# Performance work log

Measured on AMD Instinct MI355X. Metric: run time of the kernel, lower is better.

The kernel has to match this reference:

```python
import jax, jax.numpy as jnp
import numpy as np

H = W = 224
NOISE_STD = 0.45
BRIGHTNESS = 1.1          # uniform(0.8, 1.2) in original
ANGLE_DEG = 10.0          # randint(-20, 21) in original
CROP_I, CROP_J, CROP_SZ = 32, 32, 160

# Perspective: startpoints (input corners) -> endpoints (output corners).
STARTPOINTS = [[0, 0], [223, 0], [223, 223], [0, 223]]
ENDPOINTS = [[30, 20], [200, 25], [210, 200], [15, 190]]  # fixed draws within original ranges

def _perspective_coeffs(startpoints, endpoints):
    # Solve homography mapping OUTPUT coords (endpoints) -> INPUT coords (startpoints),
    # same convention as torchvision._get_perspective_coeffs(endpoints, startpoints).
    A = np.zeros((8, 8), dtype=np.float64)
    b = np.zeros((8,), dtype=np.float64)
    for k, ((xi, yi), (xo, yo)) in enumerate(zip(startpoints, endpoints)):
        A[2 * k] = [xo, yo, 1, 0, 0, 0, -xo * xi, -yo * xi]
        b[2 * k] = xi
        A[2 * k + 1] = [0, 0, 0, xo, yo, 1, -xo * yi, -yo * yi]
        b[2 * k + 1] = yi
    return np.linalg.solve(A, b)  # a,b,c,d,e,f,g,h

COEFFS = _perspective_coeffs(STARTPOINTS, ENDPOINTS)

def bilinear_sample(img, src_x, src_y):
    # img: [B,C,H,W]; src_x/src_y: [Ho,Wo] source pixel coords; zero fill outside.
    Hh, Ww = img.shape[-2], img.shape[-1]
    x0 = jnp.floor(src_x); y0 = jnp.floor(src_y)
    wx1 = src_x - x0; wx0 = 1.0 - wx1
    wy1 = src_y - y0; wy0 = 1.0 - wy1
    def gather(yi, xi):
        valid = (xi >= 0) & (xi <= Ww - 1) & (yi >= 0) & (yi <= Hh - 1)
        xc = jnp.clip(xi, 0, Ww - 1).astype(jnp.int32)
        yc = jnp.clip(yi, 0, Hh - 1).astype(jnp.int32)
        return img[:, :, yc, xc] * valid.astype(img.dtype)
    return (gather(y0, x0) * (wy0 * wx0) + gather(y0, x0 + 1) * (wy0 * wx1)
            + gather(y0 + 1, x0) * (wy1 * wx0) + gather(y0 + 1, x0 + 1) * (wy1 * wx1))

def perspective_grid():
    a, b_, c, d, e, f, g, h = [float(v) for v in COEFFS]
    yo, xo = jnp.meshgrid(jnp.arange(H, dtype=jnp.float32), jnp.arange(W, dtype=jnp.float32), indexing='ij')
    denom = g * xo + h * yo + 1.0
    return (a * xo + b_ * yo + c) / denom, (d * xo + e * yo + f) / denom

def rotate_grid(angle_deg):
    cx, cy = (W - 1) / 2.0, (H - 1) / 2.0
    t = jnp.float32(np.deg2rad(angle_deg))
    cos, sin = jnp.cos(t), jnp.sin(t)
    yo, xo = jnp.meshgrid(jnp.arange(H, dtype=jnp.float32), jnp.arange(W, dtype=jnp.float32), indexing='ij')
    dx, dy = xo - cx, yo - cy
    return cx + cos * dx + sin * dy, cy - sin * dx + cos * dy

def setup_inputs() -> dict:
    key = jax.random.key(0)
    k1, k2 = jax.random.split(key)
    x = jax.random.uniform(k1, (128, 3, H, W), dtype=jnp.float32)
    noise = jax.random.normal(k2, (128, 3, H, W), dtype=jnp.float32)
    return {"x": x, "noise": noise}

def reference(x, noise):
    # (hflip result discarded in the original -> no-op)
    x = x + NOISE_STD * noise                       # additive gaussian noise
    x = jnp.clip(x * BRIGHTNESS, 0.0, 1.0)          # adjust_brightness (float clamp to [0,1])
    px, py = perspective_grid()
    x = bilinear_sample(x, px, py)                  # perspective warp, bilinear, fill 0
    rx, ry = rotate_grid(ANGLE_DEG)
    x = bilinear_sample(x, rx, ry)                  # rotate, bilinear, fill 0
    x = x[..., CROP_I:CROP_I + CROP_SZ, CROP_J:CROP_J + CROP_SZ]  # 160x160 crop
    B, C = x.shape[0], x.shape[1]
    x = jax.image.resize(x, (B, C, H, W), method='bicubic')       # bicubic upsample back to 224
    return x
```

## Files before the change

### kernel.cpp

```cpp
#include <hip/hip_runtime.h>
#include <cmath>
#include <cstring>

#define HH 224
#define WW 224
#define CROP 160
#define CI 32
#define CJ 32
#define NCH 384
#define CH_STRIDE (HH*WW)
#define CROP_STRIDE (CROP*CROP)

#define TILE2 32
#define NTIL2 5
#define GCH2 8
#define BH2 64
#define BHCAP 62
#define NG2 18
#define BWSTR 77

#define TILE 16
#define NTIL 10
#define GCH 8
#define BMAXH 33
#define BMAXW 35
#define LROWS 35
#define LSTR  37
#define LWORDS (LROWS*LSTR)

struct AugParams {
  float a, b, c, d, e, f, g, h;
  float cosT, sinT;
};

__device__ __forceinline__ void axis_weights(int o, float w[4], int id[4]) {
  float s = (o + 0.5f) * (160.0f / 224.0f) - 0.5f;
  int base = (int)floorf(s) - 1;
  float sum = 0.0f;
#pragma unroll
  for (int t = 0; t < 4; ++t) {
    int ii = base + t;
    float dd = fabsf(s - (float)ii);
    float kw;
    if (dd < 1.0f)      kw = ((1.5f * dd - 2.5f) * dd) * dd + 1.0f;
    else if (dd < 2.0f) kw = ((-0.5f * dd + 2.5f) * dd - 4.0f) * dd + 2.0f;
    else                kw = 0.0f;
    if (ii < 0 || ii > CROP - 1) kw = 0.0f;
    w[t] = kw;
    sum += kw;
    id[t] = min(max(ii, 0), CROP - 1);
  }
  float inv = 1.0f / sum;
#pragma unroll
  for (int t = 0; t < 4; ++t) w[t] *= inv;
}

__global__ void table_kernel(float4* __restrict__ wt, int4* __restrict__ it) {
  int o = blockIdx.x * blockDim.x + threadIdx.x;
  if (o >= HH) return;
  float w[4]; int id[4];
  axis_weights(o, w, id);
  wt[o] = make_float4(w[0], w[1], w[2], w[3]);
  it[o] = make_int4(id[0], id[1], id[2], id[3]);
}

__device__ __forceinline__ float preproc(float v, float nv) {
  float p = (v + 0.45f * nv) * 1.1f;
  return fminf(fmaxf(p, 0.0f), 1.0f);
}

__device__ __forceinline__ float bf2f(unsigned short u) {
  return __uint_as_float(((unsigned int)u) << 16);
}

__global__ __launch_bounds__(256) void preproc_kernel(
    const float4* __restrict__ xin, const float4* __restrict__ nin,
    ushort4* __restrict__ pre, int n4) {
  int stride = gridDim.x * blockDim.x;
  for (int i = blockIdx.x * blockDim.x + threadIdx.x; i < n4; i += stride) {
    float4 x = xin[i];
    float4 n = nin[i];
    float p0 = preproc(x.x, n.x);
    float p1 = preproc(x.y, n.y);
    float p2 = preproc(x.z, n.z);
    float p3 = preproc(x.w, n.w);
    ushort4 o;
    unsigned int b0 = __float_as_uint(p0), b1 = __float_as_uint(p1);
    unsigned int b2 = __float_as_uint(p2), b3 = __float_as_uint(p3);
    o.x = (unsigned short)((b0 + 0x7fff + ((b0 >> 16) & 1)) >> 16);
    o.y = (unsigned short)((b1 + 0x7fff + ((b1 >> 16) & 1)) >> 16);
    o.z = (unsigned short)((b2 + 0x7fff + ((b2 >> 16) & 1)) >> 16);
    o.w = (unsigned short)((b3 + 0x7fff + ((b3 >> 16) & 1)) >> 16);
    pre[i] = o;
  }
}

__device__ __forceinline__ void make_taps(int i, int j, const AugParams P,
                                          int txs[16], int tys[16], float wts[16]) {
  const float cx = (WW - 1) * 0.5f, cy = (HH - 1) * 0.5f;
  float xr = (float)(j + CJ), yr = (float)(i + CI);
  float dx = xr - cx, dy = yr - cy;
  float rx = cx + P.cosT * dx + P.sinT * dy;
  float ry = cy - P.sinT * dx + P.cosT * dy;
  float x0f = floorf(rx), y0f = floorf(ry);
  int x0 = (int)x0f, y0 = (int)y0f;
  float wx1 = rx - x0f, wy1 = ry - y0f;
  float rwx[2] = {1.0f - wx1, wx1};
  float rwy[2] = {1.0f - wy1, wy1};
  int k = 0;
#pragma unroll
  for (int ny = 0; ny < 2; ++ny) {
#pragma unroll
    for (int nx = 0; nx < 2; ++nx) {
      int yn = y0 + ny, xn = x0 + nx;
      bool vn = (xn >= 0 && xn <= WW - 1 && yn >= 0 && yn <= HH - 1);
      float wn = rwy[ny] * rwx[nx] * (vn ? 1.0f : 0.0f);
      float xo = (float)xn, yo = (float)yn;
      float inv = 1.0f / (P.g * xo + P.h * yo + 1.0f);
      float px = (P.a * xo + P.b * yo + P.c) * inv;
      float py = (P.d * xo + P.e * yo + P.f) * inv;
      float px0f = floorf(px), py0f = floorf(py);
      int px0 = (int)px0f, py0 = (int)py0f;
      float pwx1 = px - px0f, pwy1 = py - py0f;
      float pwx[2] = {1.0f - pwx1, pwx1};
      float pwy[2] = {1.0f - pwy1, pwy1};
#pragma unroll
      for (int ty = 0; ty < 2; ++ty) {
#pragma unroll
        for (int tx = 0; tx < 2; ++tx) {
          int yt = py0 + ty, xt = px0 + tx;
          bool vt = (xt >= 0 && xt <= WW - 1 && yt >= 0 && yt <= HH - 1);
          tys[k] = min(max(yt, 0), HH - 1);
          txs[k] = min(max(xt, 0), WW - 1);
          wts[k] = wn * pwy[ty] * pwx[tx] * (vt ? 1.0f : 0.0f);
          ++k;
        }
      }
    }
  }
}

__device__ __forceinline__ void make_patches2(int i, int j, const AugParams P,
                                              int by0, int bx0e,
                                              int pofs[4], float wts[16]) {
  const float cx = (WW - 1) * 0.5f, cy = (HH - 1) * 0.5f;
  float xr = (float)(j + CJ), yr = (float)(i + CI);
  float dx = xr - cx, dy = yr - cy;
  float rx = cx + P.cosT * dx + P.sinT * dy;
  float ry = cy - P.sinT * dx + P.cosT * dy;
  float x0f = floorf(rx), y0f = floorf(ry);
  int x0 = (int)x0f, y0 = (int)y0f;
  float wx1 = rx - x0f, wy1 = ry - y0f;
  float rwx[2] = {1.0f - wx1, wx1};
  float rwy[2] = {1.0f - wy1, wy1};
  int n = 0;
#pragma unroll
  for (int ny = 0; ny < 2; ++ny) {
#pragma unroll
    for (int nx = 0; nx < 2; ++nx) {
      int yn = y0 + ny, xn = x0 + nx;
      bool vn = (xn >= 0 && xn <= WW - 1 && yn >= 0 && yn <= HH - 1);
      float wn = rwy[ny] * rwx[nx] * (vn ? 1.0f : 0.0f);
      float xo = (float)xn, yo = (float)yn;
      float inv = 1.0f / (P.g * xo + P.h * yo + 1.0f);
      float px = (P.a * xo + P.b * yo + P.c) * inv;
      float py = (P.d * xo + P.e * yo + P.f) * inv;
      float px0f = floorf(px), py0f = floorf(py);
      int px0 = (int)px0f, py0 = (int)py0f;
      float pwx1 = px - px0f, pwy1 = py - py0f;
      float pwx[2] = {1.0f - pwx1, pwx1};
      float pwy[2] = {1.0f - pwy1, pwy1};
#pragma unroll
      for (int ty = 0; ty < 2; ++ty) {
#pragma unroll
        for (int tx = 0; tx < 2; ++tx) {
          int yt = py0 + ty, xt = px0 + tx;
          bool vt = (xt >= 0 && xt <= WW - 1 && yt >= 0 && yt <= HH - 1);
          wts[n * 4 + ty * 2 + tx] = wn * pwy[ty] * pwx[tx] * (vt ? 1.0f : 0.0f);
        }
      }
      int r0 = py0 - by0 + 1;
      int c0 = px0 - bx0e + 4;
      r0 = min(max(r0, 0), BH2 - 2);
      c0 = min(max(c0, 0), BWSTR - 2);
      pofs[n] = r0 * BWSTR + c0;
      ++n;
    }
  }
}

__global__ __launch_bounds__(256, 3) void warp_pre_kernel(
    const unsigned short* __restrict__ pre, float* __restrict__ crop,
    AugParams P) {
  __shared__ float s_img[2][BH2 * BWSTR];
  int tile = blockIdx.x;
  int ch0  = blockIdx.y * GCH2;
  int i0 = (tile / NTIL2) * TILE2;
  int j0 = (tile % NTIL2) * TILE2;

  const float cx = (WW - 1) * 0.5f, cy = (HH - 1) * 0.5f;
  float rxmin = 1e30f, rxmax = -1e30f, rymin = 1e30f, rymax = -1e30f;
#pragma unroll
  for (int c = 0; c < 4; ++c) {
    float xr = (float)(j0 + CJ + ((c & 1) ? TILE2 - 1 : 0));
    float yr = (float)(i0 + CI + ((c & 2) ? TILE2 - 1 : 0));
    float dx = xr - cx, dy = yr - cy;
    float rx = cx + P.cosT * dx + P.sinT * dy;
    float ry = cy - P.sinT * dx + P.cosT * dy;
    rxmin = fminf(rxmin, rx); rxmax = fmaxf(rxmax, rx);
    rymin = fminf(rymin, ry); rymax = fmaxf(rymax, ry);
  }
  float xnlo = floorf(rxmin), xnhi = floorf(rxmax) + 1.0f;
  float ynlo = floorf(rymin), ynhi = floorf(rymax) + 1.0f;
  float pxmin = 1e30f, pxmax = -1e30f, pymin = 1e30f, pymax = -1e30f;
#pragma unroll
  for (int c = 0; c < 4; ++c) {
    float xo = (c & 1) ? xnhi : xnlo;
    float yo = (c & 2) ? ynhi : ynlo;
    float inv = 1.0f / (P.g * xo + P.h * yo + 1.0f);
    float px = (P.a * xo + P.b * yo + P.c) * inv;
    float py = (P.d * xo + P.e * yo + P.f) * inv;
    pxmin = fminf(pxmin, px); pxmax = fmaxf(pxmax, px);
    pymin = fminf(pymin, py); pymax = fmaxf(pymax, py);
  }
  int bx0 = max(0, (int)floorf(pxmin));
  int bx1 = min(WW - 1, (int)floorf(pxmax) + 1);
  int by0 = max(0, (int)floorf(pymin));
  int by1 = min(HH - 1, (int)floorf(pymax) + 1);
  int bx0e = bx0 & ~3;
  int bh = by1 - by0 + 1;
  int gmax = (bx1 - bx0e + 4) >> 2;
  bool use_lds = (bh <= BHCAP) && (gmax <= NG2 - 1);

  int tid = threadIdx.x;

  if (use_lds) {
    int pofs[4][4]; float wts[4][16];
#pragma unroll
    for (int k = 0; k < 4; ++k) {
      int p = tid + k * 256;
      make_patches2(i0 + (p >> 5), j0 + (p & 31), P, by0, bx0e, pofs[k], wts[k]);
    }

    for (int s = tid; s < 2 * BH2 * BWSTR; s += 256)
      ((float*)s_img)[s] = 0.0f;
    __syncthreads();

    int nslots = bh * NG2;
    {
      const unsigned short* pb = pre + (size_t)ch0 * CH_STRIDE;
#pragma unroll
      for (int q = 0; q < 5; ++q) {
        int s = tid + q * 256;
        if (s < nslots) {
          int r = s / NG2, g = s - r * NG2;
          int x = bx0e - 4 + g * 4;
          if (x >= 0 && g <= gmax) {
            ushort4 v = *(const ushort4*)(pb + (by0 + r) * WW + x);
            float* d = &s_img[0][(r + 1) * BWSTR + g * 4];
            d[0] = bf2f(v.x); d[1] = bf2f(v.y); d[2] = bf2f(v.z); d[3] = bf2f(v.w);
          }
        }
      }
      __syncthreads();
    }

    int buf = 0;
    for (int cc = 0; cc < GCH2; ++cc) {
      int ch = ch0 + cc;
      bool more = (cc < GCH2 - 1);
      ushort4 xv[5];
      if (more) {
        const unsigned short* pb = pre + (size_t)(ch + 1) * CH_STRIDE;
#pragma unroll
        for (int q = 0; q < 5; ++q) {
          int s = tid + q * 256;
          if (s < nslots) {
            int r = s / NG2, g = s - r * NG2;
            int x = bx0e - 4 + g * 4;
            if (x >= 0 && g <= gmax)
              xv[q] = *(const ushort4*)(pb + (by0 + r) * WW + x);
          }
        }
      }
      const float* sb = s_img[buf];
      float* cb = crop + (size_t)ch * CROP_STRIDE;
#pragma unroll
      for (int k = 0; k < 4; ++k) {
        int p = tid + k * 256;
        float acc = 0.0f;
#pragma unroll
        for (int n = 0; n < 4; ++n) {
          int o = pofs[k][n];
          float v00 = sb[o],         v01 = sb[o + 1];
          float v10 = sb[o + BWSTR], v11 = sb[o + BWSTR + 1];
          acc = fmaf(wts[k][n * 4 + 0], v00, acc);
          acc = fmaf(wts[k][n * 4 + 1], v01, acc);
          acc = fmaf(wts[k][n * 4 + 2], v10, acc);
          acc = fmaf(wts[k][n * 4 + 3], v11, acc);
        }
        cb[i0 * CROP + (p >> 5) * CROP + j0 + (p & 31)] = acc;
      }
      if (more) {
        float* sw = s_img[buf ^ 1];
#pragma unroll
        for (int q = 0; q < 5; ++q) {
          int s = tid + q * 256;
          if (s < nslots) {
            int r = s / NG2, g = s - r * NG2;
            int x = bx0e - 4 + g * 4;
            if (x >= 0 && g <= gmax) {
              float* d = &sw[(r + 1) * BWSTR + g * 4];
              d[0] = bf2f(xv[q].x); d[1] = bf2f(xv[q].y);
              d[2] = bf2f(xv[q].z); d[3] = bf2f(xv[q].w);
            }
          }
        }
      }
      __syncthreads();
      buf ^= 1;
    }
  } else {
    for (int k = 0; k < 4; ++k) {
      int p = tid + k * 256;
      int i = i0 + (p >> 5), j = j0 + (p & 31);
      int txs[16], tys[16]; float w[16];
      make_taps(i, j, P, txs, tys, w);
      for (int cc = 0; cc < GCH2; ++cc) {
        int ch = ch0 + cc;
        const unsigned short* pb = pre + (size_t)ch * CH_STRIDE;
        float acc = 0.0f;
#pragma unroll
        for (int t = 0; t < 16; ++t)
          acc = fmaf(w[t], bf2f(pb[tys[t] * WW + txs[t]]), acc);
        crop[(size_t)ch * CROP_STRIDE + i * CROP + j] = acc;
      }
    }
  }
}

__device__ __forceinline__ void make_patches(int i, int j, const AugParams P,
                                             int by0, int bx0, int bh, int bw,
                                             int pofs[4], float wts[16]) {
  const float cx = (WW - 1) * 0.5f, cy = (HH - 1) * 0.5f;
  float xr = (float)(j + CJ), yr = (float)(i + CI);
  float dx = xr - cx, dy = yr - cy;
  float rx = cx + P.cosT * dx + P.sinT * dy;
  float ry = cy - P.sinT * dx + P.cosT * dy;
  float x0f = floorf(rx), y0f = floorf(ry);
  int x0 = (int)x0f, y0 = (int)y0f;
  float wx1 = rx - x0f, wy1 = ry - y0f;
  float rwx[2] = {1.0f - wx1, wx1};
  float rwy[2] = {1.0f - wy1, wy1};
  int n = 0;
#pragma unroll
  for (int ny = 0; ny < 2; ++ny) {
#pragma unroll
    for (int nx = 0; nx < 2; ++nx) {
      int yn = y0 + ny, xn = x0 + nx;
      bool vn = (xn >= 0 && xn <= WW - 1 && yn >= 0 && yn <= HH - 1);
      float wn = rwy[ny] * rwx[nx] * (vn ? 1.0f : 0.0f);
      float xo = (float)xn, yo = (float)yn;
      float inv = 1.0f / (P.g * xo + P.h * yo + 1.0f);
      float px = (P.a * xo + P.b * yo + P.c) * inv;
      float py = (P.d * xo + P.e * yo + P.f) * inv;
      float px0f = floorf(px), py0f = floorf(py);
      int px0 = (int)px0f, py0 = (int)py0f;
      float pwx1 = px - px0f, pwy1 = py - py0f;
      float pwx[2] = {1.0f - pwx1, pwx1};
      float pwy[2] = {1.0f - pwy1, pwy1};
#pragma unroll
      for (int ty = 0; ty < 2; ++ty) {
#pragma unroll
        for (int tx = 0; tx < 2; ++tx) {
          int yt = py0 + ty, xt = px0 + tx;
          bool vt = (xt >= 0 && xt <= WW - 1 && yt >= 0 && yt <= HH - 1);
          wts[n * 4 + ty * 2 + tx] = wn * pwy[ty] * pwx[tx] * (vt ? 1.0f : 0.0f);
        }
      }
      int ly = py0 - by0;
      int lx = px0 - bx0;
      if (ly < -1 || ly > bh - 1) ly = 0;
      if (lx < -1 || lx > bw - 1) lx = 0;
      pofs[n] = (ly + 1) * LSTR + (lx + 1);
      ++n;
    }
  }
}

__global__ __launch_bounds__(256) void warp_direct_kernel(
    const float* __restrict__ xin, const float* __restrict__ nin,
    float* __restrict__ crop, AugParams P) {
  __shared__ float s_img[2][LWORDS];
  int tile = blockIdx.x;
  int ch0  = blockIdx.y * GCH;
  int i0 = (tile / NTIL) * TILE;
  int j0 = (tile % NTIL) * TILE;

  const float cx = (WW - 1) * 0.5f, cy = (HH - 1) * 0.5f;
  float rxmin = 1e30f, rxmax = -1e30f, rymin = 1e30f, rymax = -1e30f;
#pragma unroll
  for (int c = 0; c < 4; ++c) {
    float xr = (float)(j0 + CJ + ((c & 1) ? TILE - 1 : 0));
    float yr = (float)(i0 + CI + ((c & 2) ? TILE - 1 : 0));
    float dx = xr - cx, dy = yr - cy;
    float rx = cx + P.cosT * dx + P.sinT * dy;
    float ry = cy - P.sinT * dx + P.cosT * dy;
    rxmin = fminf(rxmin, rx); rxmax = fmaxf(rxmax, rx);
    rymin = fminf(rymin, ry); rymax = fmaxf(rymax, ry);
  }
  float xnlo = floorf(rxmin), xnhi = floorf(rxmax) + 1.0f;
  float ynlo = floorf(rymin), ynhi = floorf(rymax) + 1.0f;
  float pxmin = 1e30f, pxmax = -1e30f, pymin = 1e30f, pymax = -1e30f;
#pragma unroll
  for (int c = 0; c < 4; ++c) {
    float xo = (c & 1) ? xnhi : xnlo;
    float yo = (c & 2) ? ynhi : ynlo;
    float inv = 1.0f / (P.g * xo + P.h * yo + 1.0f);
    float px = (P.a * xo + P.b * yo + P.c) * inv;
    float py = (P.d * xo + P.e * yo + P.f) * inv;
    pxmin = fminf(pxmin, px); pxmax = fmaxf(pxmax, px);
    pymin = fminf(pymin, py); pymax = fmaxf(pymax, py);
  }
  int bx0 = max(0, (int)floorf(pxmin));
  int bx1 = min(WW - 1, (int)floorf(pxmax) + 1);
  int by0 = max(0, (int)floorf(pymin));
  int by1 = min(HH - 1, (int)floorf(pymax) + 1);
  int bw = bx1 - bx0 + 1;
  int bh = by1 - by0 + 1;
  bool use_lds = (bw <= BMAXW && bh <= BMAXH);

  int tid = threadIdx.x;
  int i = i0 + (tid >> 4);
  int j = j0 + (tid & 15);
  int opix = i * CROP + j;

  if (use_lds) {
    int pofs[4]; float wts[16];
    make_patches(i, j, P, by0, bx0, bh, bw, pofs, wts);
    for (int s = tid; s < 2 * LWORDS; s += 256)
      ((float*)s_img)[s] = 0.0f;
    __syncthreads();
    {
      const float* xb = xin + (size_t)ch0 * CH_STRIDE;
      const float* nb = nin + (size_t)ch0 * CH_STRIDE;
      int r = tid >> 5, c = tid & 31;
#pragma unroll
      for (int rr = 0; rr < 5; ++rr) {
        int rcur = r + rr * 8;
        if (rcur < bh && c < bw) {
          int g = (by0 + rcur) * WW + bx0 + c;
          s_img[0][(rcur + 1) * LSTR + (c + 1)] = preproc(xb[g], nb[g]);
        }
      }
      if (bw > 32) {
        int r2 = tid >> 2, c2 = 32 + (tid & 3);
        if (r2 < bh && c2 < bw) {
          int g = (by0 + r2) * WW + bx0 + c2;
          s_img[0][(r2 + 1) * LSTR + (c2 + 1)] = preproc(xb[g], nb[g]);
        }
      }
      __syncthreads();
    }
    int buf = 0;
    int r = tid >> 5, c = tid & 31;
    int r2 = tid >> 2, c2 = 32 + (tid & 3);
    for (int cc = 0; cc < GCH; ++cc) {
      int ch = ch0 + cc;
      bool more = (cc < GCH - 1);
      float xv[5], nv[5], xe = 0.0f, ne = 0.0f;
      if (more) {
        const float* xb = xin + (size_t)(ch + 1) * CH_STRIDE;
        const float* nb = nin + (size_t)(ch + 1) * CH_STRIDE;
#pragma unroll
        for (int rr = 0; rr < 5; ++rr) {
          int rcur = r + rr * 8;
          if (rcur < bh && c < bw) {
            int g = (by0 + rcur) * WW + bx0 + c;
            xv[rr] = xb[g]; nv[rr] = nb[g];
          }
        }
        if (bw > 32 && r2 < bh && c2 < bw) {
          int g = (by0 + r2) * WW + bx0 + c2;
          xe = xb[g]; ne = nb[g];
        }
      }
      const float* sb = s_img[buf];
      float acc = 0.0f;
#pragma unroll
      for (int n = 0; n < 4; ++n) {
        int p = pofs[n];
        acc = fmaf(wts[n * 4 + 0], sb[p], acc);
        acc = fmaf(wts[n * 4 + 1], sb[p + 1], acc);
        acc = fmaf(wts[n * 4 + 2], sb[p + LSTR], acc);
        acc = fmaf(wts[n * 4 + 3], sb[p + LSTR + 1], acc);
      }
      crop[(size_t)ch * CROP_STRIDE + opix] = acc;
      if (more) {
        float* sw = s_img[buf ^ 1];
#pragma unroll
        for (int rr = 0; rr < 5; ++rr) {
          int rcur = r + rr * 8;
          if (rcur < bh && c < bw)
            sw[(rcur + 1) * LSTR + (c + 1)] = preproc(xv[rr], nv[rr]);
        }
        if (bw > 32 && r2 < bh && c2 < bw)
          sw[(r2 + 1) * LSTR + (c2 + 1)] = preproc(xe, ne);
      }
      __syncthreads();
      buf ^= 1;
    }
  } else {
    int txs[16], tys[16]; float wts[16];
    make_taps(i, j, P, txs, tys, wts);
    for (int cc = 0; cc < GCH; ++cc) {
      int ch = ch0 + cc;
      const float* xb = xin + (size_t)ch * CH_STRIDE;
      const float* nb = nin + (size_t)ch * CH_STRIDE;
      float acc = 0.0f;
#pragma unroll
      for (int t = 0; t < 16; ++t) {
        int g = tys[t] * WW + txs[t];
        acc = fmaf(wts[t], preproc(xb[g], nb[g]), acc);
      }
      crop[(size_t)ch * CROP_STRIDE + opix] = acc;
    }
  }
}

#define STRIPROWS 28
#define HROWS 25
__global__ __launch_bounds__(256) void resize_strips_kernel(
    const float* __restrict__ crop, const float4* __restrict__ wt,
    const int4* __restrict__ it, float* __restrict__ out) {
  __shared__ float hbuf[HROWS * WW];
  int s = blockIdx.x;
  int ch = blockIdx.y;
  int r0 = max(0, s * 20 - 2);
  const float* cb = crop + (size_t)ch * CROP_STRIDE;
  int tid = threadIdx.x;

  for (int e = tid; e < HROWS * WW; e += 256) {
    int r = e / WW;
    int xo = e - r * WW;
    int cr = min(r0 + r, CROP - 1);
    float4 wx = wt[xo]; int4 ix = it[xo];
    const float* row = cb + cr * CROP;
    hbuf[e] = wx.x * row[ix.x] + wx.y * row[ix.y] +
              wx.z * row[ix.z] + wx.w * row[ix.w];
  }
  __syncthreads();
  for (int e = tid; e < STRIPROWS * WW; e += 256) {
    int yl = e / WW;
    int xo = e - yl * WW;
    int yo = s * STRIPROWS + yl;
    float4 wy = wt[yo]; int4 iy = it[yo];
    float o = wy.x * hbuf[(iy.x - r0) * WW + xo] +
              wy.y * hbuf[(iy.y - r0) * WW + xo] +
              wy.z * hbuf[(iy.z - r0) * WW + xo] +
              wy.w * hbuf[(iy.w - r0) * WW + xo];
    out[((size_t)ch * HH + yo) * WW + xo] = o;
  }
}

__device__ float crop_val(const float* __restrict__ xb, const float* __restrict__ nb,
                          int i, int j, AugParams P) {
  int txs[16], tys[16]; float wts[16];
  make_taps(i, j, P, txs, tys, wts);
  float acc = 0.0f;
#pragma unroll
  for (int t = 0; t < 16; ++t)
    acc = fmaf(wts[t], preproc(xb[tys[t] * WW + txs[t]], nb[tys[t] * WW + txs[t]]), acc);
  return acc;
}

__global__ __launch_bounds__(256) void fused_fallback_kernel(
    const float* __restrict__ xin, const float* __restrict__ nin,
    float* __restrict__ out, AugParams P, int total) {
  int stride = gridDim.x * blockDim.x;
  for (int idx = blockIdx.x * blockDim.x + threadIdx.x; idx < total; idx += stride) {
    int xo = idx % WW;
    int t2 = idx / WW;
    int yo = t2 % HH;
    int ch = t2 / HH;
    float wxa[4]; int ixa[4]; axis_weights(xo, wxa, ixa);
    float wya[4]; int iya[4]; axis_weights(yo, wya, iya);
    const float* xb = xin + (size_t)ch * CH_STRIDE;
    const float* nb = nin + (size_t)ch * CH_STRIDE;
    float acc = 0.0f;
#pragma unroll
    for (int ty = 0; ty < 4; ++ty)
#pragma unroll
      for (int tx = 0; tx < 4; ++tx)
        acc += wya[ty] * wxa[tx] * crop_val(xb, nb, iya[ty], ixa[tx], P);
    out[idx] = acc;
  }
}

static void solve_coeffs(double C[8]) {
  const double sp[4][2] = {{0, 0}, {223, 0}, {223, 223}, {0, 223}};
  const double ep[4][2] = {{30, 20}, {200, 25}, {210, 200}, {15, 190}};
  double A[8][9];
  for (int k = 0; k < 4; ++k) {
    double xi = sp[k][0], yi = sp[k][1], xo = ep[k][0], yo = ep[k][1];
    double r0[9] = {xo, yo, 1, 0, 0, 0, -xo * xi, -yo * xi, xi};
    double r1[9] = {0, 0, 0, xo, yo, 1, -xo * yi, -yo * yi, yi};
    std::memcpy(A[2 * k], r0, sizeof r0);
    std::memcpy(A[2 * k + 1], r1, sizeof r1);
  }
  for (int col = 0; col < 8; ++col) {
    int piv = col;
    for (int r = col + 1; r < 8; ++r)
      if (std::fabs(A[r][col]) > std::fabs(A[piv][col])) piv = r;
    if (piv != col)
      for (int cc = 0; cc < 9; ++cc) { double t = A[col][cc]; A[col][cc] = A[piv][cc]; A[piv][cc] = t; }
    double p = A[col][col];
    for (int r = 0; r < 8; ++r) {
      if (r == col) continue;
      double fmul = A[r][col] / p;
      for (int cc = col; cc < 9; ++cc) A[r][cc] -= fmul * A[col][cc];
    }
  }
  for (int r = 0; r < 8; ++r) C[r] = A[r][8] / A[r][r];
}

extern "C" void kernel_launch(void* const* d_in, const int* in_sizes, int n_in,
                              void* d_out, int out_size, void* d_ws, size_t ws_size,
                              hipStream_t stream) {
  const float* xin = (const float*)d_in[0];
  const float* nin = (const float*)d_in[1];
  float* out = (float*)d_out;

  double C[8];
  solve_coeffs(C);
  AugParams P;
  P.a = (float)C[0]; P.b = (float)C[1]; P.c = (float)C[2]; P.d = (float)C[3];
  P.e = (float)C[4]; P.f = (float)C[5]; P.g = (float)C[6]; P.h = (float)C[7];
  double t = 10.0 * M_PI / 180.0;
  P.cosT = (float)std::cos(t);
  P.sinT = (float)std::sin(t);

  const int total = NCH * HH * WW;
  const size_t PRE_BYTES = (size_t)NCH * CH_STRIDE * 2;
  const size_t CROP_BYTES = (size_t)NCH * CROP_STRIDE * 4;

  const size_t TBLW_OFF = PRE_BYTES + 256;
  const size_t TBLI_OFF = TBLW_OFF + 3584;
  const size_t CROPF_OFF = TBLI_OFF + 3584;
  const size_t need_full = CROPF_OFF + CROP_BYTES;
  const size_t need_med = 8192 + CROP_BYTES;

  if (ws_size >= need_full) {
    unsigned short* pre = (unsigned short*)d_ws;
    float4* wt = (float4*)((char*)d_ws + TBLW_OFF);
    int4*   it = (int4*)((char*)d_ws + TBLI_OFF);
    float* crop = (float*)((char*)d_ws + CROPF_OFF);

    hipLaunchKernelGGL(table_kernel, dim3(1), dim3(256), 0, stream, wt, it);
    hipLaunchKernelGGL(preproc_kernel, dim3(2048), dim3(256), 0, stream,
                       (const float4*)xin, (const float4*)nin,
                       (ushort4*)pre, total / 4);
    dim3 g1(NTIL2 * NTIL2, NCH / GCH2);
    hipLaunchKernelGGL(warp_pre_kernel, g1, dim3(256), 0, stream, pre, crop, P);
    dim3 g2(HH / STRIPROWS, NCH);
    hipLaunchKernelGGL(resize_strips_kernel, g2, dim3(256), 0, stream, crop, wt, it, out);
  } else if (ws_size >= need_med) {
    float4* wt = (float4*)d_ws;
    int4*   it = (int4*)((char*)d_ws + 3584);
    float* crop = (float*)((char*)d_ws + 8192);

    hipLaunchKernelGGL(table_kernel, dim3(1), dim3(256), 0, stream, wt, it);
    dim3 g1(NTIL * NTIL, NCH / GCH);
    hipLaunchKernelGGL(warp_direct_kernel, g1, dim3(256), 0, stream, xin, nin, crop, P);
    dim3 g2(HH / STRIPROWS, NCH);
    hipLaunchKernelGGL(resize_strips_kernel, g2, dim3(256), 0, stream, crop, wt, it, out);
  } else {
    hipLaunchKernelGGL(fused_fallback_kernel, dim3(2048), dim3(256), 0, stream,
                       xin, nin, out, P, total);
  }
}
```

Before: 126.7 us.

## Vectorize LDS stores, unroll preproc kernel, and use nontemporal output stores

The preprocessing kernel drops its grid-stride loop. Each thread now handles 16 floats with a launch grid sized exactly to the data, which assumes the total divides evenly. The shared-memory row stride is padded from 77 to 80 so the bf16-to-float expansion can be written as one aligned float4 store per slot. The final resize output is written with nontemporal stores to keep it out of the cache. Together these aim to cut instruction overhead and LDS store count, at the cost of possibly more LDS bank conflicts from the new stride.

```diff
diff --git a/kernel.cpp b/kernel.cpp
--- a/kernel.cpp
+++ b/kernel.cpp
@@ -17,7 +17,7 @@
 #define BH2 64
 #define BHCAP 62
 #define NG2 18
-#define BWSTR 77
+#define BWSTR 80
 
 #define TILE 16
 #define NTIL 10
@@ -73,26 +73,28 @@
   return __uint_as_float(((unsigned int)u) << 16);
 }
 
+__device__ __forceinline__ unsigned short f2bf(float f) {
+  unsigned int b = __float_as_uint(f);
+  return (unsigned short)((b + 0x7fff + ((b >> 16) & 1)) >> 16);
+}
+
 __global__ __launch_bounds__(256) void preproc_kernel(
     const float4* __restrict__ xin, const float4* __restrict__ nin,
-    ushort4* __restrict__ pre, int n4) {
-  int stride = gridDim.x * blockDim.x;
-  for (int i = blockIdx.x * blockDim.x + threadIdx.x; i < n4; i += stride) {
-    float4 x = xin[i];
-    float4 n = nin[i];
-    float p0 = preproc(x.x, n.x);
-    float p1 = preproc(x.y, n.y);
-    float p2 = preproc(x.z, n.z);
-    float p3 = preproc(x.w, n.w);
-    ushort4 o;
-    unsigned int b0 = __float_as_uint(p0), b1 = __float_as_uint(p1);
-    unsigned int b2 = __float_as_uint(p2), b3 = __float_as_uint(p3);
-    o.x = (unsigned short)((b0 + 0x7fff + ((b0 >> 16) & 1)) >> 16);
-    o.y = (unsigned short)((b1 + 0x7fff + ((b1 >> 16) & 1)) >> 16);
-    o.z = (unsigned short)((b2 + 0x7fff + ((b2 >> 16) & 1)) >> 16);
-    o.w = (unsigned short)((b3 + 0x7fff + ((b3 >> 16) & 1)) >> 16);
-    pre[i] = o;
-  }
+    ushort4* __restrict__ pre) {
+  int t = blockIdx.x * 256 + threadIdx.x;
+  int b = t * 4;
+  float4 x0 = xin[b + 0], x1 = xin[b + 1], x2 = xin[b + 2], x3 = xin[b + 3];
+  float4 n0 = nin[b + 0], n1 = nin[b + 1], n2 = nin[b + 2], n3 = nin[b + 3];
+  ushort4 o0, o1, o2, o3;
+  o0.x = f2bf(preproc(x0.x, n0.x)); o0.y = f2bf(preproc(x0.y, n0.y));
+  o0.z = f2bf(preproc(x0.z, n0.z)); o0.w = f2bf(preproc(x0.w, n0.w));
+  o1.x = f2bf(preproc(x1.x, n1.x)); o1.y = f2bf(preproc(x1.y, n1.y));
+  o1.z = f2bf(preproc(x1.z, n1.z)); o1.w = f2bf(preproc(x1.w, n1.w));
+  o2.x = f2bf(preproc(x2.x, n2.x)); o2.y = f2bf(preproc(x2.y, n2.y));
+  o2.z = f2bf(preproc(x2.z, n2.z)); o2.w = f2bf(preproc(x2.w, n2.w));
+  o3.x = f2bf(preproc(x3.x, n3.x)); o3.y = f2bf(preproc(x3.y, n3.y));
+  o3.z = f2bf(preproc(x3.z, n3.z)); o3.w = f2bf(preproc(x3.w, n3.w));
+  pre[b + 0] = o0; pre[b + 1] = o1; pre[b + 2] = o2; pre[b + 3] = o3;
 }
 
 __device__ __forceinline__ void make_taps(int i, int j, const AugParams P,
@@ -257,8 +259,8 @@
           int x = bx0e - 4 + g * 4;
           if (x >= 0 && g <= gmax) {
             ushort4 v = *(const ushort4*)(pb + (by0 + r) * WW + x);
-            float* d = &s_img[0][(r + 1) * BWSTR + g * 4];
-            d[0] = bf2f(v.x); d[1] = bf2f(v.y); d[2] = bf2f(v.z); d[3] = bf2f(v.w);
+            *(float4*)&s_img[0][(r + 1) * BWSTR + g * 4] =
+                make_float4(bf2f(v.x), bf2f(v.y), bf2f(v.z), bf2f(v.w));
           }
         }
       }
@@ -310,9 +312,9 @@
             int r = s / NG2, g = s - r * NG2;
             int x = bx0e - 4 + g * 4;
             if (x >= 0 && g <= gmax) {
-              float* d = &sw[(r + 1) * BWSTR + g * 4];
-              d[0] = bf2f(xv[q].x); d[1] = bf2f(xv[q].y);
-              d[2] = bf2f(xv[q].z); d[3] = bf2f(xv[q].w);
+              *(float4*)&sw[(r + 1) * BWSTR + g * 4] =
+                  make_float4(bf2f(xv[q].x), bf2f(xv[q].y),
+                              bf2f(xv[q].z), bf2f(xv[q].w));
             }
           }
         }
@@ -559,7 +561,7 @@
               wy.y * hbuf[(iy.y - r0) * WW + xo] +
               wy.z * hbuf[(iy.z - r0) * WW + xo] +
               wy.w * hbuf[(iy.w - r0) * WW + xo];
-    out[((size_t)ch * HH + yo) * WW + xo] = o;
+    __builtin_nontemporal_store(o, &out[((size_t)ch * HH + yo) * WW + xo]);
   }
 }
 
@@ -657,9 +659,8 @@
     float* crop = (float*)((char*)d_ws + CROPF_OFF);
 
     hipLaunchKernelGGL(table_kernel, dim3(1), dim3(256), 0, stream, wt, it);
-    hipLaunchKernelGGL(preproc_kernel, dim3(2048), dim3(256), 0, stream,
-                       (const float4*)xin, (const float4*)nin,
-                       (ushort4*)pre, total / 4);
+    hipLaunchKernelGGL(preproc_kernel, dim3(total / 16 / 256), dim3(256), 0, stream,
+                       (const float4*)xin, (const float4*)nin, (ushort4*)pre);
     dim3 g1(NTIL2 * NTIL2, NCH / GCH2);
     hipLaunchKernelGGL(warp_pre_kernel, g1, dim3(256), 0, stream, pre, crop, P);
     dim3 g2(HH / STRIPROWS, NCH);
```

Measured after the change: 121.0 us. 1.05x faster.
